# Kernel optimization log

Measured on AMD Instinct MI355X. Metric: run time of the kernel, lower is better.

## Reference

```python
import jax, jax.numpy as jnp
import numpy as np

T = 0.5  # moco temperature


def _normalize(x, axis):
    return x / jnp.clip(jnp.linalg.norm(x, axis=axis, keepdims=True), 1e-12)


def _balanced_bce(logits, labels):
    # BalancedCrossEntropyLoss(size_average=True): class-frequency weighted BCE-with-logits
    numel = labels.size
    num_pos = jnp.sum(labels)
    num_neg = numel - num_pos
    loss = jax.nn.softplus(-logits) * labels + jax.nn.softplus(logits) * (1.0 - labels)
    loss_pos = jnp.sum(labels * loss)
    loss_neg = jnp.sum((1.0 - labels) * loss)
    return ((num_neg / numel) * loss_pos + (num_pos / numel) * loss_neg) / numel


def setup_inputs() -> dict:
    key = jax.random.key(0)
    ks = jax.random.split(key, 4)
    B, D, H, W, K = 8, 32, 48, 48, 8192
    return {
        "q_feat": jax.random.normal(ks[0], (B, D, H, W), jnp.float32),
        "k_feat": jax.random.normal(ks[1], (B, D, H, W), jnp.float32),
        "q_bg": jax.random.normal(ks[2], (B, H, W), jnp.float32),
        "sal_q": jnp.ones((B, H, W), jnp.float32),
        "sal_k": jnp.ones((B, H, W), jnp.float32),
        "queue": jax.random.normal(ks[3], (32, K), jnp.float32),
        "num_negatives": 5,
    }


def reference(q_feat, k_feat, q_bg, sal_q, sal_k, queue, num_negatives):
    B, D, H, W = q_feat.shape
    HW = H * W
    key = jax.random.key(42)
    k_dir, k_neg = jax.random.split(key)

    # q = normalize(model_q(im_q))
    qn = _normalize(q_feat, axis=1)                            # (B,D,H,W)
    q_flat = qn.transpose(0, 2, 3, 1).reshape(-1, D)           # (B*HW, D)
    sal_loss = _balanced_bce(q_bg, sal_q)

    # batch-id per foreground pixel; with all-ones sal every pixel is foreground
    offset = jnp.arange(0, 2 * B, 2, dtype=sal_q.dtype)
    tmpv = ((sal_q + offset[:, None, None]) * sal_q).reshape(-1)
    mask_indexes = jnp.arange(B * HW)                          # nonzero() under ones-mask
    tmp = jnp.floor_divide(tmpv[mask_indexes], 2.0)

    # prototypes from key encoder (no-grad in original)
    kn = _normalize(k_feat, axis=1).reshape(B, D, HW)
    protos = jnp.einsum('bdh,bh->bd', kn, sal_k.reshape(B, HW).astype(k_feat.dtype))
    protos = _normalize(protos, axis=1)                        # (B,D)

    # random-walk positive: rejection-sampling over 4-neighborhood == uniform over
    # in-bounds neighbors; sample with masked Gumbel-argmax
    steps = jnp.array([[1, 0], [-1, 0], [0, 1], [0, -1]])
    rr, cc = jnp.meshgrid(jnp.arange(H), jnp.arange(W), indexing='ij')
    nr = rr[:, :, None] + steps[:, 0]
    nc = cc[:, :, None] + steps[:, 1]
    valid = (nr >= 0) & (nr < H) & (nc >= 0) & (nc < W)        # (H,W,4)
    g = jax.random.gumbel(k_dir, (B, H, W, 4))
    d = jnp.argmax(jnp.where(valid[None], 0.0, -jnp.inf) + g, axis=-1)  # (B,H,W)
    pr = rr[None] + steps[d, 0]
    pc = cc[None] + steps[d, 1]
    pos_idx = (pr * W + pc).reshape(B, HW)
    q_hw = qn.reshape(B, D, HW).transpose(0, 2, 1)             # (B,HW,D)
    neigh = jnp.take_along_axis(q_hw, pos_idx[:, :, None], axis=1)
    positive = jnp.sum(q_hw * neigh, axis=-1)                  # (B,HW)

    # negatives: torch.multinomial(uniform w/ self zeroed, 5, without replacement)
    # == Gumbel top-k over HW with the self index masked out
    gn = jax.random.gumbel(k_neg, (B, HW, HW))
    gn = jnp.where(jnp.eye(HW, dtype=bool)[None], -jnp.inf, gn)
    _, neg_idx = jax.lax.top_k(gn, num_negatives)              # (B,HW,nn)
    neg = q_hw[jnp.arange(B)[:, None, None], neg_idx]          # (B,HW,nn,D)
    neg_logits = jnp.einsum('bhd,bhkd->bhk', q_hw, neg)

    l_logits = jnp.concatenate([positive[..., None], neg_logits], axis=-1)
    l_logits = l_logits.reshape(B * HW, num_negatives + 1) / T
    l_labels = jnp.zeros(B * HW, jnp.float32)

    # q = index_select(q_flat, mask_indexes)  (computed but unused in original)
    _ = q_flat[mask_indexes]

    queue_n = _normalize(queue, axis=0)                        # buffer normalized at init
    l_batch = q_flat @ protos.T                                # (B*HW, B)
    l_mem = q_flat @ queue_n                                   # (B*HW, K)
    logits = jnp.concatenate([l_batch, l_mem], axis=1) / T
    return logits, tmp, l_logits, l_labels, sal_loss
```

## Files before the change

### kernel.cpp

```cpp
#include <hip/hip_runtime.h>
#include <stdint.h>

#define BB 8
#define DD 32
#define HH 48
#define WW 48
#define HWSZ 2304
#define NROW 18432
#define KQ 8192
#define NCOL 8200

#define OFF_TMP    151142400
#define OFF_LLOG   151160832
#define OFF_LLBL   151271424
#define OFF_SAL    151289856

#define N_MAIN4  6912

typedef short short8v __attribute__((ext_vector_type(8)));
typedef float float4v __attribute__((ext_vector_type(4)));

__device__ __forceinline__ uint32_t rotl_d(uint32_t x, int d){
  return __builtin_amdgcn_alignbit(x, x, (uint32_t)(32-d));
}

__device__ __forceinline__ void tf2x32(uint32_t k0, uint32_t k1, uint32_t x0, uint32_t x1,
                                       uint32_t &o0, uint32_t &o1){
  uint32_t ks2 = k0 ^ k1 ^ 0x1BD11BDAu;
  x0 += k0; x1 += k1;
  x0+=x1; x1=rotl_d(x1,13); x1^=x0;
  x0+=x1; x1=rotl_d(x1,15); x1^=x0;
  x0+=x1; x1=rotl_d(x1,26); x1^=x0;
  x0+=x1; x1=rotl_d(x1, 6); x1^=x0;
  x0+=k1; x1+=ks2+1u;
  x0+=x1; x1=rotl_d(x1,17); x1^=x0;
  x0+=x1; x1=rotl_d(x1,29); x1^=x0;
  x0+=x1; x1=rotl_d(x1,16); x1^=x0;
  x0+=x1; x1=rotl_d(x1,24); x1^=x0;
  x0+=ks2; x1+=k0+2u;
  x0+=x1; x1=rotl_d(x1,13); x1^=x0;
  x0+=x1; x1=rotl_d(x1,15); x1^=x0;
  x0+=x1; x1=rotl_d(x1,26); x1^=x0;
  x0+=x1; x1=rotl_d(x1, 6); x1^=x0;
  x0+=k0; x1+=k1+3u;
  x0+=x1; x1=rotl_d(x1,17); x1^=x0;
  x0+=x1; x1=rotl_d(x1,29); x1^=x0;
  x0+=x1; x1=rotl_d(x1,16); x1^=x0;
  x0+=x1; x1=rotl_d(x1,24); x1^=x0;
  x0+=k1; x1+=ks2+4u;
  x0+=x1; x1=rotl_d(x1,13); x1^=x0;
  x0+=x1; x1=rotl_d(x1,15); x1^=x0;
  x0+=x1; x1=rotl_d(x1,26); x1^=x0;
  x0+=x1; x1=rotl_d(x1, 6); x1^=x0;
  x0+=ks2; x1+=k0+5u;
  o0=x0; o1=x1;
}

static inline uint32_t rotl_h(uint32_t x,int d){return (x<<d)|(x>>(32-d));}
static void tf_host(uint32_t k0,uint32_t k1,uint32_t x0,uint32_t x1,uint32_t&o0,uint32_t&o1){
  uint32_t ks2=k0^k1^0x1BD11BDAu;
  x0+=k0;x1+=k1;
  const int RA[4]={13,15,26,6}, RBR[4]={17,29,16,24};
  for(int i=0;i<4;++i){x0+=x1;x1=rotl_h(x1,RA[i]);x1^=x0;}
  x0+=k1; x1+=ks2+1u;
  for(int i=0;i<4;++i){x0+=x1;x1=rotl_h(x1,RBR[i]);x1^=x0;}
  x0+=ks2; x1+=k0+2u;
  for(int i=0;i<4;++i){x0+=x1;x1=rotl_h(x1,RA[i]);x1^=x0;}
  x0+=k0; x1+=k1+3u;
  for(int i=0;i<4;++i){x0+=x1;x1=rotl_h(x1,RBR[i]);x1^=x0;}
  x0+=k1; x1+=ks2+4u;
  for(int i=0;i<4;++i){x0+=x1;x1=rotl_h(x1,RA[i]);x1^=x0;}
  x0+=ks2; x1+=k0+5u;
  o0=x0;o1=x1;
}

__device__ __forceinline__ ushort f2bf(float x){
  uint32_t u = __float_as_uint(x);
  uint32_t r = (u + 0x7FFFu + ((u>>16)&1u)) >> 16;
  return (ushort)r;
}

__global__ __launch_bounds__(256) void k_pre(const float* __restrict__ q_feat,
                                             const float* __restrict__ k_feat,
                                             const float* __restrict__ q_bg,
                                             const float* __restrict__ sal_q,
                                             const float* __restrict__ sal_k,
                                             const float* __restrict__ queue,
                                             float* __restrict__ q_flat,
                                             ushort* __restrict__ qbf,
                                             ushort* __restrict__ qnT,
                                             float* __restrict__ praw,
                                             float* __restrict__ tmp_out,
                                             float* __restrict__ lbl_out,
                                             float* __restrict__ acc){
  __shared__ float pacc[32];
  int bid = blockIdx.x;
  if (bid < 72){
    int b = bid / 9;
    int hw = (bid % 9)*256 + threadIdx.x;
    const float* src = q_feat + (size_t)b*DD*HWSZ + hw;
    float v[32]; float ss = 0.f;
#pragma unroll
    for (int d=0; d<32; ++d){ v[d] = src[(size_t)d*HWSZ]; ss += v[d]*v[d]; }
    float inv = 1.f / fmaxf(sqrtf(ss), 1e-12f);
    size_t row = (size_t)b*HWSZ + hw;
    float4* o4 = (float4*)(q_flat + row*DD);
#pragma unroll
    for (int i=0;i<8;++i)
      o4[i] = make_float4(v[4*i]*inv, v[4*i+1]*inv, v[4*i+2]*inv, v[4*i+3]*inv);
    ushort us[32];
#pragma unroll
    for (int d=0; d<32; ++d) us[d] = f2bf(v[d]*inv);
    short8v* ob = (short8v*)(qbf + row*DD);
#pragma unroll
    for (int i=0;i<4;++i) ob[i] = *(short8v*)&us[8*i];
  } else if (bid < 144){
    int rb = bid - 72;
    int b = rb / 9;
    int hw = (rb % 9)*256 + threadIdx.x;
    const float* src = k_feat + (size_t)b*DD*HWSZ + hw;
    float v[32]; float ss = 0.f;
#pragma unroll
    for (int d=0; d<32; ++d){ v[d] = src[(size_t)d*HWSZ]; ss += v[d]*v[d]; }
    float w_t = sal_k[(size_t)b*HWSZ + hw] * (1.f / fmaxf(sqrtf(ss), 1e-12f));
    if (threadIdx.x < 32) pacc[threadIdx.x] = 0.f;
    __syncthreads();
    int lane = threadIdx.x & 63;
#pragma unroll
    for (int d=0; d<32; ++d){
      float s = v[d]*w_t;
      s+=__shfl_xor(s,32,64); s+=__shfl_xor(s,16,64); s+=__shfl_xor(s,8,64);
      s+=__shfl_xor(s,4,64);  s+=__shfl_xor(s,2,64);  s+=__shfl_xor(s,1,64);
      if (lane==0) atomicAdd(&pacc[d], s);
    }
    __syncthreads();
    if (threadIdx.x < 32) atomicAdd(&praw[b*32 + threadIdx.x], pacc[threadIdx.x]);
  } else if (bid < 176){
    int j = (bid-144)*256 + threadIdx.x;
    float v[32]; float ss = 0.f;
#pragma unroll
    for (int d=0; d<DD; ++d){ v[d] = queue[(size_t)d*KQ + j]; ss += v[d]*v[d]; }
    float inv = 1.f / fmaxf(sqrtf(ss), 1e-12f);
    ushort us[32];
#pragma unroll
    for (int d=0; d<DD; ++d) us[d] = f2bf(v[d]*inv);
    short8v* ob = (short8v*)(qnT + (size_t)j*DD);
#pragma unroll
    for (int i=0;i<4;++i) ob[i] = *(short8v*)&us[8*i];
  } else {
    int i = (bid-176)*256 + threadIdx.x;
    float s = sal_q[i];
    int b = i / HWSZ;
    float tmpv = (s + 2.f*(float)b) * s;
    __builtin_nontemporal_store(floorf(tmpv * 0.5f), &tmp_out[i]);
    __builtin_nontemporal_store(0.f, &lbl_out[i]);
    float x = q_bg[i];
    float c = log1pf(expf(-fabsf(x)));
    float sp_neg = fmaxf(-x,0.f) + c;
    float sp_pos = fmaxf( x,0.f) + c;
    float loss = sp_neg*s + sp_pos*(1.f - s);
    float a0 = s, a1 = s*loss, a2 = (1.f-s)*loss;
    a0+=__shfl_xor(a0,32,64); a1+=__shfl_xor(a1,32,64); a2+=__shfl_xor(a2,32,64);
    a0+=__shfl_xor(a0,16,64); a1+=__shfl_xor(a1,16,64); a2+=__shfl_xor(a2,16,64);
    a0+=__shfl_xor(a0, 8,64); a1+=__shfl_xor(a1, 8,64); a2+=__shfl_xor(a2, 8,64);
    a0+=__shfl_xor(a0, 4,64); a1+=__shfl_xor(a1, 4,64); a2+=__shfl_xor(a2, 4,64);
    a0+=__shfl_xor(a0, 2,64); a1+=__shfl_xor(a1, 2,64); a2+=__shfl_xor(a2, 2,64);
    a0+=__shfl_xor(a0, 1,64); a1+=__shfl_xor(a1, 1,64); a2+=__shfl_xor(a2, 1,64);
    if ((threadIdx.x&63)==0){ atomicAdd(&acc[0],a0); atomicAdd(&acc[1],a1); atomicAdd(&acc[2],a2); }
  }
}

__global__ __launch_bounds__(256) void k_pnormfin(const float* __restrict__ praw, float* __restrict__ pn,
                                                  const float* __restrict__ acc, float* __restrict__ out_sal){
  int t = threadIdx.x;
  float v = praw[t];
  float ss = v*v;
  ss += __shfl_xor(ss,16,64); ss+=__shfl_xor(ss,8,64); ss+=__shfl_xor(ss,4,64);
  ss+=__shfl_xor(ss,2,64); ss+=__shfl_xor(ss,1,64);
  pn[t] = v / fmaxf(sqrtf(ss), 1e-12f);
  if (t == 0){
    float numel = (float)NROW;
    float npos = acc[0];
    float nneg = numel - npos;
    out_sal[0] = (nneg/numel*acc[1] + npos/numel*acc[2]) / numel;
  }
}

__global__ __launch_bounds__(256) void k_main(const float* __restrict__ q_flat,
                                              const ushort* __restrict__ qbf,
                                              const ushort* __restrict__ qnT,
                                              const float* __restrict__ pn,
                                              float* __restrict__ out,
                                              float* __restrict__ llog,
                                              uint32_t kd0, uint32_t kd1,
                                              uint32_t kn0, uint32_t kn1){
  __shared__ float lds[16*260];
  int bid = blockIdx.x;
  int wave = threadIdx.x>>6, lane = threadIdx.x&63;

  if ((bid % 3) == 0){
    int g = bid/3;
    int rowbase = (g>>1)*16;
    int colhalf = (g&1)*4096;
    int r16 = lane&15, hi = lane>>4, koff = hi*8;

    const short8v a = *(const short8v*)(qbf + ((size_t)(rowbase + r16))*DD + koff);

    if ((g&1)==0 && threadIdx.x < 32){
      int row = threadIdx.x >> 1, c0 = (threadIdx.x & 1)*4;
      const float* qr = q_flat + (size_t)(rowbase+row)*DD;
      float s0=0.f,s1=0.f,s2=0.f,s3=0.f;
#pragma unroll
      for (int d=0; d<32; ++d){
        float qd = qr[d];
        s0 += qd*pn[(c0+0)*32+d];
        s1 += qd*pn[(c0+1)*32+d];
        s2 += qd*pn[(c0+2)*32+d];
        s3 += qd*pn[(c0+3)*32+d];
      }
      float4v hv = {2.f*s0, 2.f*s1, 2.f*s2, 2.f*s3};
      __builtin_nontemporal_store(hv,
          (float4v*)(out + (size_t)(rowbase+row)*NCOL + c0));
    }

    for (int c=0; c<16; ++c){
      int chunkbase = colhalf + c*256;
#pragma unroll
      for (int t=0; t<4; ++t){
        int j0 = chunkbase + wave*64 + t*16;
        const short8v bfr = *(const short8v*)(qnT + ((size_t)(j0 + r16))*DD + koff);
        float4v acc = {0.f,0.f,0.f,0.f};
        acc = __builtin_amdgcn_mfma_f32_16x16x32_bf16(a, bfr, acc, 0, 0, 0);
        int ccol = wave*64 + t*16 + r16;
#pragma unroll
        for (int i=0;i<4;++i) lds[(hi*4+i)*260 + ccol] = 2.f*acc[i];
      }
      __syncthreads();
#pragma unroll
      for (int k=0;k<4;++k){
        int f = threadIdx.x + k*256;
        int row = f>>6, col4 = f&63;
        float4v v = *(const float4v*)&lds[row*260 + col4*4];
        __builtin_nontemporal_store(v,
            (float4v*)(out + (size_t)(rowbase+row)*NCOL + 8 + chunkbase + col4*4));
      }
      __syncthreads();
    }
  } else {
    int l = bid - bid/3 - 1;
    int row = l*4 + wave;
    int b = row/HWSZ, h = row%HWSZ;
    int r = h/WW, c0 = h%WW;

    uint32_t m = 0;
    if (lane < 4){
      uint32_t i = (uint32_t)row*4u + (uint32_t)lane;
      uint32_t o0,o1;
      tf2x32(kd0,kd1,0u,i,o0,o1);
      m = (o0 ^ o1) >> 9;
    }
    uint32_t mm[4];
    mm[0]=__shfl(m,0,64); mm[1]=__shfl(m,1,64); mm[2]=__shfl(m,2,64); mm[3]=__shfl(m,3,64);
    const int sr[4]={1,-1,0,0}, sc[4]={0,0,1,-1};
    int best=-1; uint32_t bv=0;
#pragma unroll
    for (int j=0;j<4;++j){
      int nr=r+sr[j], nc=c0+sc[j];
      bool ok = (nr>=0)&&(nr<HH)&&(nc>=0)&&(nc<WW);
      if (ok && (best<0 || mm[j]>bv)){ best=j; bv=mm[j]; }
    }
    int pos = (r+sr[best])*WW + (c0+sc[best]);
    int prow = b*HWSZ + pos;

    float qv = 0.f, pv = 0.f;
    if (lane<32){ qv=q_flat[(size_t)row*DD+lane]; pv=q_flat[(size_t)prow*DD+lane]; }
    float d = qv*pv;
    d+=__shfl_xor(d,16,64); d+=__shfl_xor(d,8,64); d+=__shfl_xor(d,4,64);
    d+=__shfl_xor(d,2,64); d+=__shfl_xor(d,1,64);
    if (lane==0) llog[(size_t)row*6] = 2.f*d;

    uint32_t base = (uint32_t)row * (uint32_t)HWSZ + (uint32_t)lane;
    uint32_t t0=0,t1=0,t2=0,t3=0,t4=0;
#pragma unroll 4
    for (int it=0; it<36; ++it){
      uint32_t o0,o1;
      tf2x32(kn0,kn1,0u, base + (uint32_t)(it<<6), o0,o1);
      int c = lane + (it<<6);
      uint32_t key = (((o0^o1)>>3)&0xFFFFFFC0u) | (uint32_t)(35-it);
      key = (c != h) ? key : 0u;
      uint32_t mx, mn;
      mx = t0>key?t0:key; mn = t0>key?key:t0; t0=mx; key=mn;
      mx = t1>key?t1:key; mn = t1>key?key:t1; t1=mx; key=mn;
      mx = t2>key?t2:key; mn = t2>key?key:t2; t2=mx; key=mn;
      mx = t3>key?t3:key; mn = t3>key?key:t3; t3=mx; key=mn;
      t4 = t4>key?t4:key;
    }
    int idx[5];
#pragma unroll
    for (int k=0;k<5;++k){
      uint32_t mk = t0>>6;
      int it = 35 - (int)(t0 & 63u);
      int c  = lane + (it<<6);
      unsigned long long bk = ((unsigned long long)mk<<18)
                            | ((unsigned long long)(2303-c)<<6)
                            | (unsigned long long)lane;
      #pragma unroll
      for (int o=1;o<64;o<<=1){
        unsigned long long other = __shfl_xor(bk,o,64);
        if (other > bk) bk = other;
      }
      int wl = (int)(bk & 63ull);
      idx[k] = 2303 - (int)((bk >> 6) & 0xFFFull);
      if (lane == wl){ t0=t1; t1=t2; t2=t3; t3=t4; t4=0; }
    }
#pragma unroll
    for (int k=0;k<5;++k){
      float nv = 0.f;
      if (lane < 32) nv = q_flat[(size_t)(b*HWSZ + idx[k])*DD + lane];
      float dd = qv*nv;
      dd+=__shfl_xor(dd,16,64); dd+=__shfl_xor(dd,8,64); dd+=__shfl_xor(dd,4,64);
      dd+=__shfl_xor(dd,2,64); dd+=__shfl_xor(dd,1,64);
      if (lane==0) llog[(size_t)row*6 + 1 + k] = 2.f*dd;
    }
  }
}

extern "C" void kernel_launch(void* const* d_in, const int* in_sizes, int n_in,
                              void* d_out, int out_size, void* d_ws, size_t ws_size,
                              hipStream_t stream) {
  const float* q_feat = (const float*)d_in[0];
  const float* k_feat = (const float*)d_in[1];
  const float* q_bg   = (const float*)d_in[2];
  const float* sal_q  = (const float*)d_in[3];
  const float* sal_k  = (const float*)d_in[4];
  const float* queue  = (const float*)d_in[5];
  (void)in_sizes; (void)n_in; (void)out_size; (void)ws_size;

  float* out    = (float*)d_out;
  float* logits = out;
  float* tmp    = out + OFF_TMP;
  float* llog   = out + OFF_LLOG;
  float* llbl   = out + OFF_LLBL;
  float* sal    = out + OFF_SAL;

  float* ws     = (float*)d_ws;
  float*  q_flat = ws;
  ushort* qbf    = (ushort*)(ws + 589824);
  ushort* qnT    = (ushort*)(ws + 884736);
  float*  praw   = ws + 1015808;
  float*  acc    = ws + 1016064;
  float*  pn     = ws + 1016128;

  uint32_t kd0,kd1,kn0,kn1;
  tf_host(0u,42u,0u,0u,kd0,kd1);
  tf_host(0u,42u,0u,1u,kn0,kn1);

  (void)hipMemsetAsync(praw, 0, 259*sizeof(float), stream);

  k_pre     <<<248, 256, 0, stream>>>(q_feat, k_feat, q_bg, sal_q, sal_k, queue,
                                      q_flat, qbf, qnT, praw, tmp, llbl, acc);
  k_pnormfin<<<1,   256, 0, stream>>>(praw, pn, acc, sal);
  k_main    <<<N_MAIN4, 256, 0, stream>>>(q_flat, qbf, qnT, pn, logits, llog,
                                          kd0, kd1, kn0, kn1);
}
```

Measured before the change: 182.4 us.

## Fold prototype norm and saliency loss into main kernel, split logits GEMM into quarters

```diff
diff --git a/kernel.cpp b/kernel.cpp
--- a/kernel.cpp
+++ b/kernel.cpp
@@ -15,7 +15,7 @@
 #define OFF_LLBL   151271424
 #define OFF_SAL    151289856
 
-#define N_MAIN4  6912
+#define N_MAIN5  (72 + 9216)
 
 typedef short short8v __attribute__((ext_vector_type(8)));
 typedef float float4v __attribute__((ext_vector_type(4)));
@@ -82,17 +82,12 @@
 
 __global__ __launch_bounds__(256) void k_pre(const float* __restrict__ q_feat,
                                              const float* __restrict__ k_feat,
-                                             const float* __restrict__ q_bg,
-                                             const float* __restrict__ sal_q,
                                              const float* __restrict__ sal_k,
                                              const float* __restrict__ queue,
                                              float* __restrict__ q_flat,
                                              ushort* __restrict__ qbf,
                                              ushort* __restrict__ qnT,
-                                             float* __restrict__ praw,
-                                             float* __restrict__ tmp_out,
-                                             float* __restrict__ lbl_out,
-                                             float* __restrict__ acc){
+                                             float* __restrict__ praw){
   __shared__ float pacc[32];
   int bid = blockIdx.x;
   if (bid < 72){
@@ -135,7 +130,7 @@
     }
     __syncthreads();
     if (threadIdx.x < 32) atomicAdd(&praw[b*32 + threadIdx.x], pacc[threadIdx.x]);
-  } else if (bid < 176){
+  } else {
     int j = (bid-144)*256 + threadIdx.x;
     float v[32]; float ss = 0.f;
 #pragma unroll
@@ -147,8 +142,29 @@
     short8v* ob = (short8v*)(qnT + (size_t)j*DD);
 #pragma unroll
     for (int i=0;i<4;++i) ob[i] = *(short8v*)&us[8*i];
-  } else {
-    int i = (bid-176)*256 + threadIdx.x;
+  }
+}
+
+__global__ __launch_bounds__(256) void k_main(const float* __restrict__ q_flat,
+                                              const ushort* __restrict__ qbf,
+                                              const ushort* __restrict__ qnT,
+                                              const float* __restrict__ praw,
+                                              const float* __restrict__ q_bg,
+                                              const float* __restrict__ sal_q,
+                                              float* __restrict__ out,
+                                              float* __restrict__ llog,
+                                              float* __restrict__ tmp_out,
+                                              float* __restrict__ lbl_out,
+                                              float* __restrict__ sal_out,
+                                              float* __restrict__ acc,
+                                              uint32_t kd0, uint32_t kd1,
+                                              uint32_t kn0, uint32_t kn1){
+  __shared__ float lds[16*260];
+  int bid = blockIdx.x;
+  int wave = threadIdx.x>>6, lane = threadIdx.x&63;
+
+  if (bid < 72){
+    int i = bid*256 + threadIdx.x;
     float s = sal_q[i];
     int b = i / HWSZ;
     float tmpv = (s + 2.f*(float)b) * s;
@@ -167,73 +183,56 @@
     a0+=__shfl_xor(a0, 2,64); a1+=__shfl_xor(a1, 2,64); a2+=__shfl_xor(a2, 2,64);
     a0+=__shfl_xor(a0, 1,64); a1+=__shfl_xor(a1, 1,64); a2+=__shfl_xor(a2, 1,64);
     if ((threadIdx.x&63)==0){ atomicAdd(&acc[0],a0); atomicAdd(&acc[1],a1); atomicAdd(&acc[2],a2); }
-  }
-}
-
-__global__ __launch_bounds__(256) void k_pnormfin(const float* __restrict__ praw, float* __restrict__ pn,
-                                                  const float* __restrict__ acc, float* __restrict__ out_sal){
-  int t = threadIdx.x;
-  float v = praw[t];
-  float ss = v*v;
-  ss += __shfl_xor(ss,16,64); ss+=__shfl_xor(ss,8,64); ss+=__shfl_xor(ss,4,64);
-  ss+=__shfl_xor(ss,2,64); ss+=__shfl_xor(ss,1,64);
-  pn[t] = v / fmaxf(sqrtf(ss), 1e-12f);
-  if (t == 0){
-    float numel = (float)NROW;
-    float npos = acc[0];
-    float nneg = numel - npos;
-    out_sal[0] = (nneg/numel*acc[1] + npos/numel*acc[2]) / numel;
-  }
-}
-
-__global__ __launch_bounds__(256) void k_main(const float* __restrict__ q_flat,
-                                              const ushort* __restrict__ qbf,
-                                              const ushort* __restrict__ qnT,
-                                              const float* __restrict__ pn,
-                                              float* __restrict__ out,
-                                              float* __restrict__ llog,
-                                              uint32_t kd0, uint32_t kd1,
-                                              uint32_t kn0, uint32_t kn1){
-  __shared__ float lds[16*260];
-  int bid = blockIdx.x;
-  int wave = threadIdx.x>>6, lane = threadIdx.x&63;
-
-  if ((bid % 3) == 0){
-    int g = bid/3;
-    int rowbase = (g>>1)*16;
-    int colhalf = (g&1)*4096;
+    __syncthreads();
+    if (threadIdx.x==0){
+      __threadfence();
+      uint32_t done = atomicAdd((uint32_t*)&acc[3], 1u);
+      if (done == 71u){
+        __threadfence();
+        float numel = (float)NROW;
+        float npos = acc[0];
+        float nneg = numel - npos;
+        sal_out[0] = (nneg/numel*acc[1] + npos/numel*acc[2]) / numel;
+      }
+    }
+  } else if (((bid-72) & 1) == 0){
+    int g = (bid-72)>>1;
+    int rowbase = (g>>2)*16;
+    int colq = (g&3)*2048;
     int r16 = lane&15, hi = lane>>4, koff = hi*8;
 
     const short8v a = *(const short8v*)(qbf + ((size_t)(rowbase + r16))*DD + koff);
 
-    if ((g&1)==0 && threadIdx.x < 32){
+    if ((g&3)==0 && threadIdx.x < 32){
       int row = threadIdx.x >> 1, c0 = (threadIdx.x & 1)*4;
       const float* qr = q_flat + (size_t)(rowbase+row)*DD;
       float s0=0.f,s1=0.f,s2=0.f,s3=0.f;
+      float n0=0.f,n1=0.f,n2=0.f,n3=0.f;
 #pragma unroll
       for (int d=0; d<32; ++d){
         float qd = qr[d];
-        s0 += qd*pn[(c0+0)*32+d];
-        s1 += qd*pn[(c0+1)*32+d];
-        s2 += qd*pn[(c0+2)*32+d];
-        s3 += qd*pn[(c0+3)*32+d];
-      }
-      float4v hv = {2.f*s0, 2.f*s1, 2.f*s2, 2.f*s3};
+        float p0=praw[(c0+0)*32+d], p1=praw[(c0+1)*32+d];
+        float p2=praw[(c0+2)*32+d], p3=praw[(c0+3)*32+d];
+        s0 += qd*p0; s1 += qd*p1; s2 += qd*p2; s3 += qd*p3;
+        n0 += p0*p0; n1 += p1*p1; n2 += p2*p2; n3 += p3*p3;
+      }
+      float4v hv = {2.f*s0/fmaxf(sqrtf(n0),1e-12f), 2.f*s1/fmaxf(sqrtf(n1),1e-12f),
+                    2.f*s2/fmaxf(sqrtf(n2),1e-12f), 2.f*s3/fmaxf(sqrtf(n3),1e-12f)};
       __builtin_nontemporal_store(hv,
           (float4v*)(out + (size_t)(rowbase+row)*NCOL + c0));
     }
 
-    for (int c=0; c<16; ++c){
-      int chunkbase = colhalf + c*256;
+    for (int c=0; c<8; ++c){
+      int chunkbase = colq + c*256;
 #pragma unroll
       for (int t=0; t<4; ++t){
         int j0 = chunkbase + wave*64 + t*16;
         const short8v bfr = *(const short8v*)(qnT + ((size_t)(j0 + r16))*DD + koff);
-        float4v acc = {0.f,0.f,0.f,0.f};
-        acc = __builtin_amdgcn_mfma_f32_16x16x32_bf16(a, bfr, acc, 0, 0, 0);
+        float4v acc4 = {0.f,0.f,0.f,0.f};
+        acc4 = __builtin_amdgcn_mfma_f32_16x16x32_bf16(a, bfr, acc4, 0, 0, 0);
         int ccol = wave*64 + t*16 + r16;
 #pragma unroll
-        for (int i=0;i<4;++i) lds[(hi*4+i)*260 + ccol] = 2.f*acc[i];
+        for (int i=0;i<4;++i) lds[(hi*4+i)*260 + ccol] = 2.f*acc4[i];
       }
       __syncthreads();
 #pragma unroll
@@ -247,7 +246,7 @@
       __syncthreads();
     }
   } else {
-    int l = bid - bid/3 - 1;
+    int l = (bid-72)>>1;
     int row = l*4 + wave;
     int b = row/HWSZ, h = row%HWSZ;
     int r = h/WW, c0 = h%WW;
@@ -349,17 +348,16 @@
   ushort* qnT    = (ushort*)(ws + 884736);
   float*  praw   = ws + 1015808;
   float*  acc    = ws + 1016064;
-  float*  pn     = ws + 1016128;
 
   uint32_t kd0,kd1,kn0,kn1;
   tf_host(0u,42u,0u,0u,kd0,kd1);
   tf_host(0u,42u,0u,1u,kn0,kn1);
 
-  (void)hipMemsetAsync(praw, 0, 259*sizeof(float), stream);
-
-  k_pre     <<<248, 256, 0, stream>>>(q_feat, k_feat, q_bg, sal_q, sal_k, queue,
-                                      q_flat, qbf, qnT, praw, tmp, llbl, acc);
-  k_pnormfin<<<1,   256, 0, stream>>>(praw, pn, acc, sal);
-  k_main    <<<N_MAIN4, 256, 0, stream>>>(q_flat, qbf, qnT, pn, logits, llog,
-                                          kd0, kd1, kn0, kn1);
-}
+  (void)hipMemsetAsync(praw, 0, 260*sizeof(float), stream);
+
+  k_pre <<<176, 256, 0, stream>>>(q_feat, k_feat, sal_k, queue,
+                                  q_flat, qbf, qnT, praw);
+  k_main<<<N_MAIN5, 256, 0, stream>>>(q_flat, qbf, qnT, praw, q_bg, sal_q,
+                                      logits, llog, tmp, llbl, sal, acc,
+                                      kd0, kd1, kn0, kn1);
+}
```

After: 276.0 us. +51.3%, slower.
